# Optimization experiments

Hardware: AMD Instinct MI355X
Metric: run time of the kernel (lower is better)

The kernel has to match this reference:

```python
import jax, jax.numpy as jnp
import numpy as np

EPS = 1e-7
MAX_NORM = 1.0 - 1e-5  # Poincare ball projection radius (c=1)
N_NODES, N_EDGES, N_GRAPHS = 50000, 1200000, 128
D_IN, D_H, D_OUT = 32, 64, 10


def _norm(x):
    return jnp.linalg.norm(x, axis=-1, keepdims=True).clip(EPS)


def proj(x):
    # clip points back inside the unit ball
    n = _norm(x)
    return jnp.where(n > MAX_NORM, x * (MAX_NORM / n), x)


def expmap0(u):
    # exponential map at the origin of the Poincare ball (c=1)
    n = _norm(u)
    return jnp.tanh(n) * u / n


def logmap0(x):
    # log map at the origin
    n = _norm(x).clip(EPS, MAX_NORM)
    return jnp.arctanh(n) * x / n


def segment_mean(vals, ids, num_segments):
    s = jax.ops.segment_sum(vals, ids, num_segments=num_segments)
    c = jax.ops.segment_sum(jnp.ones((vals.shape[0], 1), vals.dtype), ids, num_segments=num_segments)
    return s / jnp.maximum(c, 1.0)


def hgcn_layer(x, src, dst, W, b, act):
    # HGCN layer: logmap -> linear(+bias) in tangent space -> neighborhood mean agg -> act -> expmap -> proj
    h = logmap0(x) @ W + b                      # [N, d_out] tangent features
    msg = h[src]                                # gather over edges [E, d_out]
    h = segment_mean(msg, dst, N_NODES)         # scatter-mean aggregation
    if act is not None:
        h = act(h)
    return proj(expmap0(h))


def setup_inputs() -> dict:
    key = jax.random.key(0)
    ks = jax.random.split(key, 8)
    x = 0.1 * jax.random.normal(ks[0], (N_NODES, D_IN), dtype=jnp.float32)
    edge_index = jax.random.randint(ks[1], (2, N_EDGES), 0, N_NODES, dtype=jnp.int64)
    batch = jnp.sort(jax.random.randint(ks[2], (N_NODES,), 0, N_GRAPHS, dtype=jnp.int64))
    def glorot(k, fi, fo):
        return jax.random.normal(k, (fi, fo), dtype=jnp.float32) * np.sqrt(2.0 / (fi + fo))
    return {
        "x": x, "edge_index": edge_index, "batch": batch,
        "W1": glorot(ks[3], D_IN, D_H), "b1": jnp.zeros((D_H,), jnp.float32),
        "W2": glorot(ks[4], D_H, D_H), "b2": jnp.zeros((D_H,), jnp.float32),
        "W3": glorot(ks[5], D_H, D_H), "b3": jnp.zeros((D_H,), jnp.float32),
        "Wl": glorot(ks[6], D_H, D_OUT), "bl": jnp.zeros((D_OUT,), jnp.float32),
    }


def reference(x, edge_index, batch, W1, b1, W2, b2, W3, b3, Wl, bl):
    src, dst = edge_index[0], edge_index[1]
    lrelu = lambda t: jax.nn.leaky_relu(t, 0.2)
    h = proj(expmap0(x))
    h = hgcn_layer(h, src, dst, W1, b1, lrelu)
    h = hgcn_layer(h, src, dst, W2, b2, lrelu)
    h = hgcn_layer(h, src, dst, W3, b3, None)
    t = logmap0(h)
    pooled = segment_mean(t, batch, N_GRAPHS)    # global_mean_pool [G, D_H]
    # dropout p=0.5 inactive in eval mode
    z = proj(expmap0(pooled))
    z = logmap0(z) @ Wl + bl                     # HNN linear in tangent space
    return proj(expmap0(z))                      # [G, D_OUT]
```

## Files before the change

kernel.cpp:

```cpp
#include <hip/hip_runtime.h>
#include <hip/hip_fp16.h>
#include <hip/hip_fp8.h>
#include <math.h>

#define N_NODES 50000
#define N_EDGES 1200000
#define N_GRAPHS 128
#define D_IN 32
#define D_H 64
#define D_OUT 10
#define ELL_CAP 64

#define EPS 1e-7f
#define MAX_NORM (1.0f - 1e-5f)
#define TCLIP 6.1030335f
#define T8SCALE 16.0f

#define HB 512
#define CHUNK ((N_EDGES + HB - 1) / HB)
#define NBUCK ((N_NODES + 63) / 64)

typedef _Float16 half8 __attribute__((ext_vector_type(8)));
typedef float float4v __attribute__((ext_vector_type(4)));


__device__ __forceinline__ float wave_reduce_sum(float v) {
    #pragma unroll
    for (int off = 32; off > 0; off >>= 1)
        v += __shfl_xor(v, off, 64);
    return v;
}

__device__ __forceinline__ float reduce32(float v) {
    #pragma unroll
    for (int off = 16; off > 0; off >>= 1)
        v += __shfl_xor(v, off, 64);
    return v;
}

__device__ __forceinline__ float epl_clip64(float m) {
    float n = sqrtf(wave_reduce_sum(m * m));
    float sc = (n > TCLIP) ? (TCLIP / n) : 1.0f;
    return m * sc;
}

__device__ __forceinline__ float2 fp8x2_to_f2(ushort v) {
    __hip_fp8_e4m3 a, b;
    a.__x = (__hip_fp8_storage_t)(v & 0xff);
    b.__x = (__hip_fp8_storage_t)(v >> 8);
    return make_float2((float)a, (float)b);
}


__global__ void partsort_kernel(const int* __restrict__ src, const int* __restrict__ dst,
                                unsigned* __restrict__ sorted, int* __restrict__ rowOffs,
                                const float* __restrict__ x, __half* __restrict__ u0) {
    __shared__ int hist[1024];
    __shared__ int wsum[256];
    if (blockIdx.x >= HB) {
        int gid = (blockIdx.x - HB) * 256 + threadIdx.x;
        int node = gid >> 6;
        int lane = gid & 63;
        if (node >= N_NODES) return;
        float m = (lane < D_IN) ? x[node * D_IN + lane] : 0.0f;
        float t = epl_clip64(m);
        if (lane < D_IN) u0[node * D_IN + lane] = __float2half(t);
        return;
    }
    int i = blockIdx.x;
    int e0 = i * CHUNK;
    int e1 = min(e0 + CHUNK, N_EDGES);

    for (int t = threadIdx.x; t < 1024; t += 256) hist[t] = 0;
    __syncthreads();
    for (int e = e0 + threadIdx.x; e < e1; e += 256) {
        int d = dst[e];
        d = min(max(d, 0), N_NODES - 1);
        atomicAdd(&hist[d >> 6], 1);
    }
    __syncthreads();
    int t = threadIdx.x;
    int a0 = hist[4 * t], a1 = hist[4 * t + 1], a2 = hist[4 * t + 2], a3 = hist[4 * t + 3];
    int s01 = a0 + a1;
    int s = s01 + a2 + a3;
    wsum[t] = s;
    __syncthreads();
    for (int off = 1; off < 256; off <<= 1) {
        int v = (t >= off) ? wsum[t - off] : 0;
        __syncthreads();
        wsum[t] += v;
        __syncthreads();
    }
    int base = wsum[t] - s;
    hist[4 * t]     = base;
    hist[4 * t + 1] = base + a0;
    hist[4 * t + 2] = base + s01;
    hist[4 * t + 3] = base + s01 + a2;
    __syncthreads();
    for (int jj = threadIdx.x; jj <= NBUCK; jj += 256)
        rowOffs[i * (NBUCK + 1) + jj] = hist[jj];
    __syncthreads();
    for (int e = e0 + threadIdx.x; e < e1; e += 256) {
        int s_ = src[e];
        int d  = dst[e];
        s_ = min(max(s_, 0), N_NODES - 1);
        d  = min(max(d,  0), N_NODES - 1);
        int pos = atomicAdd(&hist[d >> 6], 1);
        sorted[(size_t)i * CHUNK + pos] = ((unsigned)d << 16) | (unsigned)s_;
    }
}

__global__ void ellbuild_kernel(const unsigned* __restrict__ sorted, const int* __restrict__ rowOffs,
                                int* __restrict__ deg, ushort* __restrict__ ell) {
    __shared__ int cnt[64];
    int j = blockIdx.x;
    if (threadIdx.x < 64) cnt[threadIdx.x] = 0;
    __syncthreads();
    for (int i = threadIdx.x; i < HB; i += 256) {
        int b0 = rowOffs[i * (NBUCK + 1) + j];
        int b1 = rowOffs[i * (NBUCK + 1) + j + 1];
        const unsigned* sp = sorted + (size_t)i * CHUNK;
        for (int e = b0; e < b1; ++e) {
            unsigned p = sp[e];
            int dl = (int)(p >> 16) & 63;
            int pos = atomicAdd(&cnt[dl], 1);
            if (pos < ELL_CAP)
                ell[(size_t)((j << 6) + dl) * ELL_CAP + pos] = (ushort)(p & 0xffffu);
        }
    }
    __syncthreads();
    int node = (j << 6) + threadIdx.x;
    if (threadIdx.x < 64 && node < N_NODES) deg[node] = cnt[threadIdx.x];
}

template <int K>
__global__ void repack_kernel(const float* __restrict__ W, __half* __restrict__ Whf) {
    const int NF = K / 32;
    int idx = blockIdx.x * 256 + threadIdx.x;
    if (idx >= 4 * NF * 64 * 8) return;
    int j = idx & 7;
    int lane = (idx >> 3) & 63;
    int f = (idx >> 9) % NF;
    int jb = (idx >> 9) / NF;
    int k = f * 32 + ((lane >> 4) * 8) + j;
    int n = jb * 16 + (lane & 15);
    Whf[idx] = __float2half(W[k * 64 + n]);
}

__global__ void meangather_kernel(const __half* __restrict__ u0, const int* __restrict__ deg,
                                  const ushort* __restrict__ ell, __half* __restrict__ m0) {
    int widx = threadIdx.x >> 6;
    int lane = threadIdx.x & 63;
    int node = blockIdx.x * 4 + widx;
    if (node >= N_NODES) return;
    int quad = lane >> 4;
    int p = lane & 15;
    int dt = deg[node];
    int d = min(dt, ELL_CAP);
    int id = (lane < d) ? (int)ell[node * ELL_CAP + lane] : 0;
    const __half2* u2 = (const __half2*)u0;

    float ax = 0.f, ay = 0.f;
    int e = 0;
    for (; e + 16 <= d; e += 16) {
        int sA0 = __shfl(id, e,      64), sB0 = __shfl(id, e + 1,  64);
        int sC0 = __shfl(id, e + 2,  64), sD0 = __shfl(id, e + 3,  64);
        int sA1 = __shfl(id, e + 4,  64), sB1 = __shfl(id, e + 5,  64);
        int sC1 = __shfl(id, e + 6,  64), sD1 = __shfl(id, e + 7,  64);
        int sA2 = __shfl(id, e + 8,  64), sB2 = __shfl(id, e + 9,  64);
        int sC2 = __shfl(id, e + 10, 64), sD2 = __shfl(id, e + 11, 64);
        int sA3 = __shfl(id, e + 12, 64), sB3 = __shfl(id, e + 13, 64);
        int sC3 = __shfl(id, e + 14, 64), sD3 = __shfl(id, e + 15, 64);
        int t0 = (quad & 1) ? sB0 : sA0, v0 = (quad & 1) ? sD0 : sC0;
        int t1 = (quad & 1) ? sB1 : sA1, v1 = (quad & 1) ? sD1 : sC1;
        int t2_ = (quad & 1) ? sB2 : sA2, v2 = (quad & 1) ? sD2 : sC2;
        int t3 = (quad & 1) ? sB3 : sA3, v3 = (quad & 1) ? sD3 : sC3;
        int s0 = (quad & 2) ? v0 : t0;
        int s1 = (quad & 2) ? v1 : t1;
        int s2 = (quad & 2) ? v2 : t2_;
        int s3 = (quad & 2) ? v3 : t3;
        float2 f0 = __half22float2(u2[s0 * 16 + p]);
        float2 f1 = __half22float2(u2[s1 * 16 + p]);
        float2 f2 = __half22float2(u2[s2 * 16 + p]);
        float2 f3 = __half22float2(u2[s3 * 16 + p]);
        ax += (f0.x + f1.x) + (f2.x + f3.x);
        ay += (f0.y + f1.y) + (f2.y + f3.y);
    }
    if (e + 4 <= d) {
        do {
            int sA = __shfl(id, e, 64), sB = __shfl(id, e + 1, 64);
            int sC = __shfl(id, e + 2, 64), sD = __shfl(id, e + 3, 64);
            int tt = (quad & 1) ? sB : sA, vv = (quad & 1) ? sD : sC;
            int s = (quad & 2) ? vv : tt;
            float2 f = __half22float2(u2[s * 16 + p]);
            ax += f.x; ay += f.y;
            e += 4;
        } while (e + 4 <= d);
    }
    for (; e < d; ++e) {
        int s = __shfl(id, e, 64);
        if (quad == 0) {
            float2 f = __half22float2(u2[s * 16 + p]);
            ax += f.x; ay += f.y;
        }
    }
    ax += __shfl_xor(ax, 16, 64); ax += __shfl_xor(ax, 32, 64);
    ay += __shfl_xor(ay, 16, 64); ay += __shfl_xor(ay, 32, 64);

    float inv = 1.0f / fmaxf((float)dt, 1.0f);
    if (quad == 0)
        ((__half2*)m0)[node * 16 + p] = __floats2half2_rn(ax * inv, ay * inv);
}

__global__ void gemmepi_kernel(const __half* __restrict__ m0, const __half* __restrict__ Whf,
                               const float* __restrict__ b, const int* __restrict__ deg,
                               __half* __restrict__ uout) {
    int gw = blockIdx.x * 4 + (threadIdx.x >> 6);
    int lane = threadIdx.x & 63;
    int node0 = gw * 16;
    if (node0 >= N_NODES) return;
    int m = lane & 15, quad = lane >> 4;

    half8 a = *(const half8*)(m0 + (size_t)(node0 + m) * 32 + quad * 8);
    float h[4][4];
    #pragma unroll
    for (int jb = 0; jb < 4; ++jb) {
        float4v acc = {0.f, 0.f, 0.f, 0.f};
        half8 bb = ((const half8*)Whf)[jb * 64 + lane];
        acc = __builtin_amdgcn_mfma_f32_16x16x32_f16(a, bb, acc, 0, 0, 0);
        float bias = b[jb * 16 + m];
        #pragma unroll
        for (int r = 0; r < 4; ++r) h[jb][r] = acc[r] + bias;
    }
    #pragma unroll
    for (int r = 0; r < 4; ++r) {
        int node = node0 + quad * 4 + r;
        int dt = deg[node];
        float nr = 0.f;
        #pragma unroll
        for (int jb = 0; jb < 4; ++jb) {
            float v = (dt == 0) ? 0.f : h[jb][r];
            v = (v >= 0.f) ? v : 0.2f * v;
            h[jb][r] = v;
            nr += v * v;
        }
        nr += __shfl_xor(nr, 1, 64); nr += __shfl_xor(nr, 2, 64);
        nr += __shfl_xor(nr, 4, 64); nr += __shfl_xor(nr, 8, 64);
        float n = sqrtf(nr);
        float sc = (n > TCLIP) ? (TCLIP / n) : 1.0f;
        #pragma unroll
        for (int jb = 0; jb < 4; ++jb)
            uout[node * 64 + jb * 16 + m] = __float2half(h[jb][r] * sc);
    }
}

template <int K>
__global__ void gemm_kernel(const __half* __restrict__ u, const __half* __restrict__ Whf,
                            const float* __restrict__ b, __hip_fp8_e4m3* __restrict__ t8) {
    const int NF = K / 32;
    int gw = blockIdx.x * 4 + (threadIdx.x >> 6);
    int lane = threadIdx.x & 63;
    int jb = gw & 3;
    int tile = gw >> 2;
    int node0 = tile * 16;
    if (node0 >= N_NODES) return;
    int m = lane & 15, quad = lane >> 4;

    float4v acc = {0.f, 0.f, 0.f, 0.f};
    const half8* bfr = (const half8*)Whf + (size_t)(jb * NF) * 64 + lane;
    #pragma unroll
    for (int f = 0; f < NF; ++f) {
        half8 a = *(const half8*)(u + (size_t)(node0 + m) * K + f * 32 + quad * 8);
        half8 bb = bfr[f * 64];
        acc = __builtin_amdgcn_mfma_f32_16x16x32_f16(a, bb, acc, 0, 0, 0);
    }
    int j = jb * 16 + m;
    float bias = b[j];
    #pragma unroll
    for (int r = 0; r < 4; ++r) {
        int node = node0 + quad * 4 + r;
        t8[node * 64 + j] = __hip_fp8_e4m3((acc[r] + bias) * T8SCALE);
    }
}

template <int ACT, int POOL>
__global__ void agg_kernel(const __hip_fp8_e4m3* __restrict__ t8, const int* __restrict__ deg,
                           const ushort* __restrict__ ell, __half* __restrict__ uout,
                           const int* __restrict__ batch, float* __restrict__ pooled,
                           float* __restrict__ cntg) {
    __shared__ float rs[4][64];
    __shared__ int gs[4];
    int widx = threadIdx.x >> 6;
    int lane = threadIdx.x & 63;
    int node = blockIdx.x * 4 + widx;
    if (node >= N_NODES) return;
    bool lo = lane < 32;
    int d2 = lane & 31;
    int dt = deg[node];
    int d = min(dt, ELL_CAP);
    int id = (lane < d) ? (int)ell[node * ELL_CAP + lane] : 0;
    const ushort* t2 = (const ushort*)t8;

    float ax = 0.f, ay = 0.f;
    int e = 0;
    for (; e + 16 <= d; e += 16) {
        int sA0 = __shfl(id, e,      64), sB0 = __shfl(id, e + 1,  64);
        int sA1 = __shfl(id, e + 2,  64), sB1 = __shfl(id, e + 3,  64);
        int sA2 = __shfl(id, e + 4,  64), sB2 = __shfl(id, e + 5,  64);
        int sA3 = __shfl(id, e + 6,  64), sB3 = __shfl(id, e + 7,  64);
        int sA4 = __shfl(id, e + 8,  64), sB4 = __shfl(id, e + 9,  64);
        int sA5 = __shfl(id, e + 10, 64), sB5 = __shfl(id, e + 11, 64);
        int sA6 = __shfl(id, e + 12, 64), sB6 = __shfl(id, e + 13, 64);
        int sA7 = __shfl(id, e + 14, 64), sB7 = __shfl(id, e + 15, 64);
        int s0 = lo ? sA0 : sB0;
        int s1 = lo ? sA1 : sB1;
        int s2 = lo ? sA2 : sB2;
        int s3 = lo ? sA3 : sB3;
        int s4 = lo ? sA4 : sB4;
        int s5 = lo ? sA5 : sB5;
        int s6 = lo ? sA6 : sB6;
        int s7 = lo ? sA7 : sB7;
        ushort w0 = t2[s0 * 32 + d2];
        ushort w1 = t2[s1 * 32 + d2];
        ushort w2 = t2[s2 * 32 + d2];
        ushort w3 = t2[s3 * 32 + d2];
        ushort w4 = t2[s4 * 32 + d2];
        ushort w5 = t2[s5 * 32 + d2];
        ushort w6 = t2[s6 * 32 + d2];
        ushort w7 = t2[s7 * 32 + d2];
        float2 f0 = fp8x2_to_f2(w0);
        float2 f1 = fp8x2_to_f2(w1);
        float2 f2 = fp8x2_to_f2(w2);
        float2 f3 = fp8x2_to_f2(w3);
        float2 f4 = fp8x2_to_f2(w4);
        float2 f5 = fp8x2_to_f2(w5);
        float2 f6 = fp8x2_to_f2(w6);
        float2 f7 = fp8x2_to_f2(w7);
        ax += ((f0.x + f1.x) + (f2.x + f3.x)) + ((f4.x + f5.x) + (f6.x + f7.x));
        ay += ((f0.y + f1.y) + (f2.y + f3.y)) + ((f4.y + f5.y) + (f6.y + f7.y));
    }
    if (e + 8 <= d) {
        int sA0 = __shfl(id, e,     64), sB0 = __shfl(id, e + 1, 64);
        int sA1 = __shfl(id, e + 2, 64), sB1 = __shfl(id, e + 3, 64);
        int sA2 = __shfl(id, e + 4, 64), sB2 = __shfl(id, e + 5, 64);
        int sA3 = __shfl(id, e + 6, 64), sB3 = __shfl(id, e + 7, 64);
        int s0 = lo ? sA0 : sB0;
        int s1 = lo ? sA1 : sB1;
        int s2 = lo ? sA2 : sB2;
        int s3 = lo ? sA3 : sB3;
        float2 f0 = fp8x2_to_f2(t2[s0 * 32 + d2]);
        float2 f1 = fp8x2_to_f2(t2[s1 * 32 + d2]);
        float2 f2 = fp8x2_to_f2(t2[s2 * 32 + d2]);
        float2 f3 = fp8x2_to_f2(t2[s3 * 32 + d2]);
        ax += (f0.x + f1.x) + (f2.x + f3.x);
        ay += (f0.y + f1.y) + (f2.y + f3.y);
        e += 8;
    }
    for (; e + 2 <= d; e += 2) {
        int sA = __shfl(id, e, 64), sB = __shfl(id, e + 1, 64);
        int s = lo ? sA : sB;
        float2 f = fp8x2_to_f2(t2[s * 32 + d2]);
        ax += f.x; ay += f.y;
    }
    if (e < d) {
        int s = __shfl(id, e, 64);
        if (lo) {
            float2 f = fp8x2_to_f2(t2[s * 32 + d2]);
            ax += f.x; ay += f.y;
        }
    }
    ax += __shfl_xor(ax, 32, 64);
    ay += __shfl_xor(ay, 32, 64);

    float inv = 1.0f / (T8SCALE * fmaxf((float)dt, 1.0f));
    float mx = ax * inv, my = ay * inv;
    if (ACT) {
        mx = (mx >= 0.f) ? mx : 0.2f * mx;
        my = (my >= 0.f) ? my : 0.2f * my;
    }
    float n = sqrtf(reduce32(mx * mx + my * my));
    float sc = (n > TCLIP) ? (TCLIP / n) : 1.0f;
    float rx = mx * sc, ry = my * sc;

    if (POOL) {
        int g = min(max(batch[node], 0), N_GRAPHS - 1);
        if (lo) { rs[widx][2 * d2] = rx; rs[widx][2 * d2 + 1] = ry; }
        if (lane == 0) gs[widx] = g;
        __syncthreads();
        int g0 = gs[0], g1 = gs[1], g2 = gs[2], g3 = gs[3];
        bool uni = (g0 == g1) && (g1 == g2) && (g2 == g3);
        if (uni) {
            if (widx == 0) {
                float sum = rs[0][lane] + rs[1][lane] + rs[2][lane] + rs[3][lane];
                atomicAdd(&pooled[g0 * 64 + lane], sum);
                if (lane == 0) atomicAdd(&cntg[g0], 4.0f);
            }
        } else {
            if (lo) {
                atomicAdd(&pooled[g * 64 + 2 * d2], rx);
                atomicAdd(&pooled[g * 64 + 2 * d2 + 1], ry);
            }
            if (lane == 0) atomicAdd(&cntg[g], 1.0f);
        }
    } else {
        if (lo) ((__half2*)uout)[node * 32 + d2] = __floats2half2_rn(rx, ry);
    }
}

__global__ void head_kernel(const float* __restrict__ pooled, const float* __restrict__ cntg,
                            const float* __restrict__ Wl, const float* __restrict__ bl,
                            float* __restrict__ out) {
    int g = blockIdx.x;
    int lane = threadIdx.x;
    float m = pooled[g * 64 + lane] / fmaxf(cntg[g], 1.0f);
    float z = epl_clip64(m);
    float acc = 0.0f;
    #pragma unroll
    for (int k = 0; k < 64; ++k) {
        float zk = __shfl(z, k, 64);
        if (lane < D_OUT) acc = fmaf(zk, Wl[k * D_OUT + lane], acc);
    }
    float o = (lane < D_OUT) ? (acc + bl[lane]) : 0.0f;
    float n = fmaxf(sqrtf(wave_reduce_sum(o * o)), EPS);
    float v = tanhf(n) * o / n;
    float nv = fmaxf(sqrtf(wave_reduce_sum(v * v)), EPS);
    if (nv > MAX_NORM) v = v * (MAX_NORM / nv);
    if (lane < D_OUT) out[g * D_OUT + lane] = v;
}


extern "C" void kernel_launch(void* const* d_in, const int* in_sizes, int n_in,
                              void* d_out, int out_size, void* d_ws, size_t ws_size,
                              hipStream_t stream) {
    const float* x   = (const float*)d_in[0];
    const int* edge  = (const int*)d_in[1];
    const int* batch = (const int*)d_in[2];
    const float* W1  = (const float*)d_in[3];
    const float* b1  = (const float*)d_in[4];
    const float* W2  = (const float*)d_in[5];
    const float* b2  = (const float*)d_in[6];
    const float* W3  = (const float*)d_in[7];
    const float* b3  = (const float*)d_in[8];
    const float* Wl  = (const float*)d_in[9];
    const float* bl  = (const float*)d_in[10];
    float* out = (float*)d_out;

    const int N = N_NODES, E = N_EDGES, G = N_GRAPHS;
    const int* src = edge;
    const int* dst = edge + E;

    char* ws = (char*)d_ws;
    int*    deg    = (int*)ws;
    float*  pooled = (float*)(deg + N);
    float*  cntg   = pooled + (size_t)G * 64;
    ushort* ell    = (ushort*)(cntg + G);
    __half* u0h    = (__half*)(ell + (size_t)N * ELL_CAP);
    __half* u1h    = u0h + (size_t)N * 32;
    __half* u2h    = u1h + (size_t)N * 64;
    __hip_fp8_e4m3* t8 = (__hip_fp8_e4m3*)(u2h + (size_t)N * 64);
    __half* m0h    = (__half*)((char*)t8 + (size_t)N * 64);
    __half* Wh1    = m0h + (size_t)N * 32;
    __half* Wh2    = Wh1 + 2048;
    __half* Wh3    = Wh2 + 4096;

    unsigned* sortedbuf = (unsigned*)u2h;
    int*      rowOffs   = (int*)t8;

    hipMemsetAsync(pooled, 0, ((size_t)G * 64 + G) * 4, stream);

    int blocksN64 = (N * 64 + 255) / 256;
    int blocksG   = 3125;
    int blocksT   = (3125 + 3) / 4;

    repack_kernel<32><<<8,  256, 0, stream>>>(W1, Wh1);
    repack_kernel<64><<<16, 256, 0, stream>>>(W2, Wh2);
    repack_kernel<64><<<16, 256, 0, stream>>>(W3, Wh3);

    partsort_kernel<<<HB + blocksN64, 256, 0, stream>>>(src, dst, sortedbuf, rowOffs, x, u0h);
    ellbuild_kernel<<<NBUCK, 256, 0, stream>>>(sortedbuf, rowOffs, deg, ell);

    meangather_kernel<<<blocksN64, 256, 0, stream>>>(u0h, deg, ell, m0h);
    gemmepi_kernel<<<blocksT, 256, 0, stream>>>(m0h, Wh1, b1, deg, u1h);

    gemm_kernel<64><<<blocksG, 256, 0, stream>>>(u1h, Wh2, b2, t8);
    agg_kernel<1, 0><<<blocksN64, 256, 0, stream>>>(t8, deg, ell, u2h, nullptr, nullptr, nullptr);
    gemm_kernel<64><<<blocksG, 256, 0, stream>>>(u2h, Wh3, b3, t8);
    agg_kernel<0, 1><<<blocksN64, 256, 0, stream>>>(t8, deg, ell, nullptr, batch, pooled, cntg);

    head_kernel<<<G, 64, 0, stream>>>(pooled, cntg, Wl, bl, out);
}
```

Measured before the change: 271.8 us.

## Gather neighbor rows with 8-byte loads and 8 edges per wave step

Both the mean-gather and aggregation kernels now split each wave into 8 groups of 8 lanes. Each lane loads 8 bytes of a neighbor row, so one wave step covers 8 edges. All up-to-64 neighbor loads are issued in a fully unrolled batch before accumulating, with cross-group shuffle reductions at the end. This replaces narrow 2-byte and 4-byte loads with a loop per edge, and is meant to raise memory-level parallelism and cut instruction count. In exchange it uses more registers per lane and adds reduction shuffles, and the 8 feature outputs per lane now need a short norm reduction and a wider store.

```diff
diff --git a/kernel.cpp b/kernel.cpp
--- a/kernel.cpp
+++ b/kernel.cpp
@@ -27,13 +27,6 @@
 __device__ __forceinline__ float wave_reduce_sum(float v) {
     #pragma unroll
     for (int off = 32; off > 0; off >>= 1)
-        v += __shfl_xor(v, off, 64);
-    return v;
-}
-
-__device__ __forceinline__ float reduce32(float v) {
-    #pragma unroll
-    for (int off = 16; off > 0; off >>= 1)
         v += __shfl_xor(v, off, 64);
     return v;
 }
@@ -153,63 +146,53 @@
     int lane = threadIdx.x & 63;
     int node = blockIdx.x * 4 + widx;
     if (node >= N_NODES) return;
-    int quad = lane >> 4;
-    int p = lane & 15;
+    int g = lane >> 3;
+    int d8 = lane & 7;
     int dt = deg[node];
     int d = min(dt, ELL_CAP);
     int id = (lane < d) ? (int)ell[node * ELL_CAP + lane] : 0;
-    const __half2* u2 = (const __half2*)u0;
-
-    float ax = 0.f, ay = 0.f;
-    int e = 0;
-    for (; e + 16 <= d; e += 16) {
-        int sA0 = __shfl(id, e,      64), sB0 = __shfl(id, e + 1,  64);
-        int sC0 = __shfl(id, e + 2,  64), sD0 = __shfl(id, e + 3,  64);
-        int sA1 = __shfl(id, e + 4,  64), sB1 = __shfl(id, e + 5,  64);
-        int sC1 = __shfl(id, e + 6,  64), sD1 = __shfl(id, e + 7,  64);
-        int sA2 = __shfl(id, e + 8,  64), sB2 = __shfl(id, e + 9,  64);
-        int sC2 = __shfl(id, e + 10, 64), sD2 = __shfl(id, e + 11, 64);
-        int sA3 = __shfl(id, e + 12, 64), sB3 = __shfl(id, e + 13, 64);
-        int sC3 = __shfl(id, e + 14, 64), sD3 = __shfl(id, e + 15, 64);
-        int t0 = (quad & 1) ? sB0 : sA0, v0 = (quad & 1) ? sD0 : sC0;
-        int t1 = (quad & 1) ? sB1 : sA1, v1 = (quad & 1) ? sD1 : sC1;
-        int t2_ = (quad & 1) ? sB2 : sA2, v2 = (quad & 1) ? sD2 : sC2;
-        int t3 = (quad & 1) ? sB3 : sA3, v3 = (quad & 1) ? sD3 : sC3;
-        int s0 = (quad & 2) ? v0 : t0;
-        int s1 = (quad & 2) ? v1 : t1;
-        int s2 = (quad & 2) ? v2 : t2_;
-        int s3 = (quad & 2) ? v3 : t3;
-        float2 f0 = __half22float2(u2[s0 * 16 + p]);
-        float2 f1 = __half22float2(u2[s1 * 16 + p]);
-        float2 f2 = __half22float2(u2[s2 * 16 + p]);
-        float2 f3 = __half22float2(u2[s3 * 16 + p]);
-        ax += (f0.x + f1.x) + (f2.x + f3.x);
-        ay += (f0.y + f1.y) + (f2.y + f3.y);
-    }
-    if (e + 4 <= d) {
-        do {
-            int sA = __shfl(id, e, 64), sB = __shfl(id, e + 1, 64);
-            int sC = __shfl(id, e + 2, 64), sD = __shfl(id, e + 3, 64);
-            int tt = (quad & 1) ? sB : sA, vv = (quad & 1) ? sD : sC;
-            int s = (quad & 2) ? vv : tt;
-            float2 f = __half22float2(u2[s * 16 + p]);
-            ax += f.x; ay += f.y;
-            e += 4;
-        } while (e + 4 <= d);
-    }
-    for (; e < d; ++e) {
-        int s = __shfl(id, e, 64);
-        if (quad == 0) {
-            float2 f = __half22float2(u2[s * 16 + p]);
-            ax += f.x; ay += f.y;
-        }
-    }
-    ax += __shfl_xor(ax, 16, 64); ax += __shfl_xor(ax, 32, 64);
-    ay += __shfl_xor(ay, 16, 64); ay += __shfl_xor(ay, 32, 64);
-
+    const char* base = (const char*)u0;
+
+    int sidx[8];
+    #pragma unroll
+    for (int i = 0; i < 8; ++i)
+        sidx[i] = __shfl(id, i * 8 + g, 64);
+
+    uint2 v[8];
+    #pragma unroll
+    for (int i = 0; i < 8; ++i)
+        if (i * 8 < d)
+            v[i] = *(const uint2*)(base + ((size_t)sidx[i] << 6) + (d8 << 3));
+
+    float a0 = 0.f, a1 = 0.f, a2 = 0.f, a3 = 0.f;
+    #pragma unroll
+    for (int i = 0; i < 8; ++i) {
+        if (i * 8 < d) {
+            float w = ((i * 8 + g) < d) ? 1.0f : 0.0f;
+            float2 f0 = __half22float2(*reinterpret_cast<const __half2*>(&v[i].x));
+            float2 f1 = __half22float2(*reinterpret_cast<const __half2*>(&v[i].y));
+            a0 = fmaf(f0.x, w, a0);
+            a1 = fmaf(f0.y, w, a1);
+            a2 = fmaf(f1.x, w, a2);
+            a3 = fmaf(f1.y, w, a3);
+        }
+    }
+    #pragma unroll
+    for (int off = 8; off <= 32; off <<= 1) {
+        a0 += __shfl_xor(a0, off, 64);
+        a1 += __shfl_xor(a1, off, 64);
+        a2 += __shfl_xor(a2, off, 64);
+        a3 += __shfl_xor(a3, off, 64);
+    }
     float inv = 1.0f / fmaxf((float)dt, 1.0f);
-    if (quad == 0)
-        ((__half2*)m0)[node * 16 + p] = __floats2half2_rn(ax * inv, ay * inv);
+    if (g == 0) {
+        __half2 h0 = __floats2half2_rn(a0 * inv, a1 * inv);
+        __half2 h1 = __floats2half2_rn(a2 * inv, a3 * inv);
+        uint2 pk;
+        pk.x = *reinterpret_cast<uint*>(&h0);
+        pk.y = *reinterpret_cast<uint*>(&h1);
+        *(uint2*)((char*)m0 + ((size_t)node << 6) + (d8 << 3)) = pk;
+    }
 }
 
 __global__ void gemmepi_kernel(const __half* __restrict__ m0, const __half* __restrict__ Whf,
@@ -294,98 +277,76 @@
     int lane = threadIdx.x & 63;
     int node = blockIdx.x * 4 + widx;
     if (node >= N_NODES) return;
-    bool lo = lane < 32;
-    int d2 = lane & 31;
+    int g = lane >> 3;
+    int d8 = lane & 7;
     int dt = deg[node];
     int d = min(dt, ELL_CAP);
     int id = (lane < d) ? (int)ell[node * ELL_CAP + lane] : 0;
-    const ushort* t2 = (const ushort*)t8;
-
-    float ax = 0.f, ay = 0.f;
-    int e = 0;
-    for (; e + 16 <= d; e += 16) {
-        int sA0 = __shfl(id, e,      64), sB0 = __shfl(id, e + 1,  64);
-        int sA1 = __shfl(id, e + 2,  64), sB1 = __shfl(id, e + 3,  64);
-        int sA2 = __shfl(id, e + 4,  64), sB2 = __shfl(id, e + 5,  64);
-        int sA3 = __shfl(id, e + 6,  64), sB3 = __shfl(id, e + 7,  64);
-        int sA4 = __shfl(id, e + 8,  64), sB4 = __shfl(id, e + 9,  64);
-        int sA5 = __shfl(id, e + 10, 64), sB5 = __shfl(id, e + 11, 64);
-        int sA6 = __shfl(id, e + 12, 64), sB6 = __shfl(id, e + 13, 64);
-        int sA7 = __shfl(id, e + 14, 64), sB7 = __shfl(id, e + 15, 64);
-        int s0 = lo ? sA0 : sB0;
-        int s1 = lo ? sA1 : sB1;
-        int s2 = lo ? sA2 : sB2;
-        int s3 = lo ? sA3 : sB3;
-        int s4 = lo ? sA4 : sB4;
-        int s5 = lo ? sA5 : sB5;
-        int s6 = lo ? sA6 : sB6;
-        int s7 = lo ? sA7 : sB7;
-        ushort w0 = t2[s0 * 32 + d2];
-        ushort w1 = t2[s1 * 32 + d2];
-        ushort w2 = t2[s2 * 32 + d2];
-        ushort w3 = t2[s3 * 32 + d2];
-        ushort w4 = t2[s4 * 32 + d2];
-        ushort w5 = t2[s5 * 32 + d2];
-        ushort w6 = t2[s6 * 32 + d2];
-        ushort w7 = t2[s7 * 32 + d2];
-        float2 f0 = fp8x2_to_f2(w0);
-        float2 f1 = fp8x2_to_f2(w1);
-        float2 f2 = fp8x2_to_f2(w2);
-        float2 f3 = fp8x2_to_f2(w3);
-        float2 f4 = fp8x2_to_f2(w4);
-        float2 f5 = fp8x2_to_f2(w5);
-        float2 f6 = fp8x2_to_f2(w6);
-        float2 f7 = fp8x2_to_f2(w7);
-        ax += ((f0.x + f1.x) + (f2.x + f3.x)) + ((f4.x + f5.x) + (f6.x + f7.x));
-        ay += ((f0.y + f1.y) + (f2.y + f3.y)) + ((f4.y + f5.y) + (f6.y + f7.y));
-    }
-    if (e + 8 <= d) {
-        int sA0 = __shfl(id, e,     64), sB0 = __shfl(id, e + 1, 64);
-        int sA1 = __shfl(id, e + 2, 64), sB1 = __shfl(id, e + 3, 64);
-        int sA2 = __shfl(id, e + 4, 64), sB2 = __shfl(id, e + 5, 64);
-        int sA3 = __shfl(id, e + 6, 64), sB3 = __shfl(id, e + 7, 64);
-        int s0 = lo ? sA0 : sB0;
-        int s1 = lo ? sA1 : sB1;
-        int s2 = lo ? sA2 : sB2;
-        int s3 = lo ? sA3 : sB3;
-        float2 f0 = fp8x2_to_f2(t2[s0 * 32 + d2]);
-        float2 f1 = fp8x2_to_f2(t2[s1 * 32 + d2]);
-        float2 f2 = fp8x2_to_f2(t2[s2 * 32 + d2]);
-        float2 f3 = fp8x2_to_f2(t2[s3 * 32 + d2]);
-        ax += (f0.x + f1.x) + (f2.x + f3.x);
-        ay += (f0.y + f1.y) + (f2.y + f3.y);
-        e += 8;
-    }
-    for (; e + 2 <= d; e += 2) {
-        int sA = __shfl(id, e, 64), sB = __shfl(id, e + 1, 64);
-        int s = lo ? sA : sB;
-        float2 f = fp8x2_to_f2(t2[s * 32 + d2]);
-        ax += f.x; ay += f.y;
-    }
-    if (e < d) {
-        int s = __shfl(id, e, 64);
-        if (lo) {
-            float2 f = fp8x2_to_f2(t2[s * 32 + d2]);
-            ax += f.x; ay += f.y;
-        }
-    }
-    ax += __shfl_xor(ax, 32, 64);
-    ay += __shfl_xor(ay, 32, 64);
+    const char* base = (const char*)t8;
+
+    int sidx[8];
+    #pragma unroll
+    for (int i = 0; i < 8; ++i)
+        sidx[i] = __shfl(id, i * 8 + g, 64);
+
+    uint2 v[8];
+    #pragma unroll
+    for (int i = 0; i < 8; ++i)
+        if (i * 8 < d)
+            v[i] = *(const uint2*)(base + ((size_t)sidx[i] << 6) + (d8 << 3));
+
+    float acc[8] = {0.f, 0.f, 0.f, 0.f, 0.f, 0.f, 0.f, 0.f};
+    #pragma unroll
+    for (int i = 0; i < 8; ++i) {
+        if (i * 8 < d) {
+            float w = ((i * 8 + g) < d) ? 1.0f : 0.0f;
+            uint lo_ = v[i].x, hi_ = v[i].y;
+            float2 f0 = fp8x2_to_f2((ushort)(lo_ & 0xffffu));
+            float2 f1 = fp8x2_to_f2((ushort)(lo_ >> 16));
+            float2 f2 = fp8x2_to_f2((ushort)(hi_ & 0xffffu));
+            float2 f3 = fp8x2_to_f2((ushort)(hi_ >> 16));
+            acc[0] = fmaf(f0.x, w, acc[0]);
+            acc[1] = fmaf(f0.y, w, acc[1]);
+            acc[2] = fmaf(f1.x, w, acc[2]);
+            acc[3] = fmaf(f1.y, w, acc[3]);
+            acc[4] = fmaf(f2.x, w, acc[4]);
+            acc[5] = fmaf(f2.y, w, acc[5]);
+            acc[6] = fmaf(f3.x, w, acc[6]);
+            acc[7] = fmaf(f3.y, w, acc[7]);
+        }
+    }
+    #pragma unroll
+    for (int j = 0; j < 8; ++j) {
+        acc[j] += __shfl_xor(acc[j], 8, 64);
+        acc[j] += __shfl_xor(acc[j], 16, 64);
+        acc[j] += __shfl_xor(acc[j], 32, 64);
+    }
 
     float inv = 1.0f / (T8SCALE * fmaxf((float)dt, 1.0f));
-    float mx = ax * inv, my = ay * inv;
-    if (ACT) {
-        mx = (mx >= 0.f) ? mx : 0.2f * mx;
-        my = (my >= 0.f) ? my : 0.2f * my;
-    }
-    float n = sqrtf(reduce32(mx * mx + my * my));
+    float val[8];
+    float nr = 0.f;
+    #pragma unroll
+    for (int j = 0; j < 8; ++j) {
+        float m = acc[j] * inv;
+        if (ACT) m = (m >= 0.f) ? m : 0.2f * m;
+        val[j] = m;
+        nr = fmaf(m, m, nr);
+    }
+    nr += __shfl_xor(nr, 1, 64);
+    nr += __shfl_xor(nr, 2, 64);
+    nr += __shfl_xor(nr, 4, 64);
+    float n = sqrtf(nr);
     float sc = (n > TCLIP) ? (TCLIP / n) : 1.0f;
-    float rx = mx * sc, ry = my * sc;
+    #pragma unroll
+    for (int j = 0; j < 8; ++j) val[j] *= sc;
 
     if (POOL) {
-        int g = min(max(batch[node], 0), N_GRAPHS - 1);
-        if (lo) { rs[widx][2 * d2] = rx; rs[widx][2 * d2 + 1] = ry; }
-        if (lane == 0) gs[widx] = g;
+        int gi = min(max(batch[node], 0), N_GRAPHS - 1);
+        if (g == 0) {
+            #pragma unroll
+            for (int j = 0; j < 8; ++j) rs[widx][d8 * 8 + j] = val[j];
+        }
+        if (lane == 0) gs[widx] = gi;
         __syncthreads();
         int g0 = gs[0], g1 = gs[1], g2 = gs[2], g3 = gs[3];
         bool uni = (g0 == g1) && (g1 == g2) && (g2 == g3);
@@ -396,14 +357,20 @@
                 if (lane == 0) atomicAdd(&cntg[g0], 4.0f);
             }
         } else {
-            if (lo) {
-                atomicAdd(&pooled[g * 64 + 2 * d2], rx);
-                atomicAdd(&pooled[g * 64 + 2 * d2 + 1], ry);
+            if (g == 0) {
+                #pragma unroll
+                for (int j = 0; j < 8; ++j)
+                    atomicAdd(&pooled[gi * 64 + d8 * 8 + j], val[j]);
             }
-            if (lane == 0) atomicAdd(&cntg[g], 1.0f);
+            if (lane == 0) atomicAdd(&cntg[gi], 1.0f);
         }
     } else {
-        if (lo) ((__half2*)uout)[node * 32 + d2] = __floats2half2_rn(rx, ry);
+        if (g == 0) {
+            half8 hv;
+            #pragma unroll
+            for (int j = 0; j < 8; ++j) hv[j] = (_Float16)val[j];
+            *(half8*)((char*)uout + ((size_t)node << 7) + (d8 << 4)) = hv;
+        }
     }
 }
 
```

New measurement: 267.1 us. About the same (-1.7%).
